# Optimization experiments

Hardware: AMD Instinct MI355X
Metric: run time of the kernel (lower is better)

The kernel has to match this reference:

```python
import jax, jax.numpy as jnp
import numpy as np
import math

B, S, E, H = 2, 2048, 1024, 16
D = E // H
# neuromodulator levels (deterministic branch choices)
NA, ACH, DA = 0.5, 0.5, -0.5

def setup_inputs() -> dict:
    key = jax.random.key(0)
    ks = jax.random.split(key, 12)
    xav = lambda k, i, o: jax.random.uniform(k, (i, o), jnp.float32, -1.0, 1.0) * math.sqrt(6.0 / (i + o))
    return {
        'query': jax.random.normal(ks[0], (B, S, E), jnp.float32),
        'key':   jax.random.normal(ks[1], (B, S, E), jnp.float32),
        'value': jax.random.normal(ks[2], (B, S, E), jnp.float32),
        'Wq': xav(ks[3], E, E), 'bq': jnp.zeros((E,), jnp.float32),
        'Wk': xav(ks[4], E, E), 'bk': jnp.zeros((E,), jnp.float32),
        'Wv': xav(ks[5], E, E), 'bv': jnp.zeros((E,), jnp.float32),
        'Wo': xav(ks[6], E, E), 'bo': jnp.zeros((E,), jnp.float32),
        'time_scales': jnp.ones((H,), jnp.float32),
    }

def reference(query, key, value, Wq, bq, Wk, bk, Wv, bv, Wo, bo, time_scales):
    # projections -> [B, H, S, D]
    q = (query @ Wq + bq).reshape(B, S, H, D).transpose(0, 2, 1, 3)
    k = (key   @ Wk + bk).reshape(B, S, H, D).transpose(0, 2, 1, 3)
    v = (value @ Wv + bv).reshape(B, S, H, D).transpose(0, 2, 1, 3)
    # per-head time-scale on keys
    k = k * time_scales[None, :, None, None]
    scores = jnp.einsum('bhtd,bhsd->bhts', q, k) / math.sqrt(D)
    # noradrenaline: temperature scaling
    temperature = 1.0 / (1.0 + NA * 0.5)
    scores = scores / temperature
    # acetylcholine: boost diagonal
    diag = jnp.eye(S, dtype=scores.dtype)[None, None]
    scores = scores * (1.0 + ACH * 0.3 * diag)
    kk = max(1, int(S * 0.2))
    topv = jax.lax.top_k(scores, kk)[0]          # [B,H,S,kk]
    min_topk = topv[..., -1:]                     # kth largest
    mask = (scores >= min_topk).astype(scores.dtype)
    scores = scores * (1.0 + (-DA) * 0.3 * mask)
    attn = jax.nn.softmax(scores, axis=-1)
    out = jnp.einsum('bhts,bhsd->bhtd', attn, v)
    out = out.transpose(0, 2, 1, 3).reshape(B, S, E)
    out = out @ Wo + bo
    return out
```

## Files before the change

### kernel.cpp

```cpp
#include <hip/hip_runtime.h>
#include <cstdint>
#include <cstddef>

#define BB 2
#define SS 2048
#define EE 1024
#define HH 16
#define DH 64
#define KKSEL 409
#define QT 16
#define PST 136

typedef __attribute__((ext_vector_type(8))) short bf16x8;
typedef __attribute__((ext_vector_type(4))) float f32x4;
typedef unsigned short ushort_t;

__device__ __forceinline__ unsigned short f2bf(float f){
    unsigned u = __float_as_uint(f);
    u += 0x7fffu + ((u >> 16) & 1u);
    return (unsigned short)(u >> 16);
}
__device__ __forceinline__ float bf2f(unsigned short h){
    return __uint_as_float(((unsigned)h) << 16);
}
__device__ __forceinline__ unsigned sortkey(float f){
    unsigned u = __float_as_uint(f);
    return (u & 0x80000000u) ? ~u : (u | 0x80000000u);
}
__device__ __forceinline__ float inv_sortkey(unsigned k){
    unsigned u = (k & 0x80000000u) ? (k & 0x7fffffffu) : ~k;
    return __uint_as_float(u);
}
__device__ __forceinline__ void split8(const float* f, bf16x8& h, bf16x8& l){
    #pragma unroll
    for (int j = 0; j < 8; ++j){
        ushort_t hh = f2bf(f[j]);
        h[j] = (short)hh;
        l[j] = (short)f2bf(f[j] - bf2f(hh));
    }
}

__global__ __launch_bounds__(256) void convert_wt(const float* __restrict__ W,
                                                  ushort_t* __restrict__ Ht,
                                                  ushort_t* __restrict__ Lt)
{
    __shared__ float T[64][65];
    const int tid = threadIdx.x;
    const int ty = tid >> 4, tx = tid & 15;
    const int n0 = blockIdx.x * 64, k0 = blockIdx.y * 64;
    #pragma unroll
    for (int i = 0; i < 4; ++i){
        const int kl = ty + i * 16;
        float4 w = *(const float4*)&W[(size_t)(k0 + kl) * EE + n0 + tx * 4];
        T[kl][tx*4 + 0] = w.x; T[kl][tx*4 + 1] = w.y;
        T[kl][tx*4 + 2] = w.z; T[kl][tx*4 + 3] = w.w;
    }
    __syncthreads();
    #pragma unroll
    for (int i = 0; i < 4; ++i){
        const int nl = ty + i * 16;
        ushort4 h, l;
        ushort_t* hp = &h.x; ushort_t* lp = &l.x;
        #pragma unroll
        for (int j = 0; j < 4; ++j){
            const float v = T[tx*4 + j][nl];
            ushort_t hh = f2bf(v);
            hp[j] = hh;
            lp[j] = f2bf(v - bf2f(hh));
        }
        const size_t o = (size_t)(n0 + nl) * EE + k0 + tx * 4;
        *(ushort4*)&Ht[o] = h;
        *(ushort4*)&Lt[o] = l;
    }
}

template<int MODE>
__global__ __launch_bounds__(256) void gemm_mfma(
        const float* __restrict__ X,
        const ushort_t* __restrict__ Wth, const ushort_t* __restrict__ Wtl,
        const float* __restrict__ bias, const float* __restrict__ ts,
        float* __restrict__ OutF, ushort_t* __restrict__ OutH,
        ushort_t* __restrict__ OutL)
{
    __shared__ ushort_t buf[2][16384];
    const int tid  = threadIdx.x;
    const int lane = tid & 63, wave = tid >> 6;
    const int c16  = lane & 15, qd = lane >> 4;
    const int m0 = blockIdx.y * 128, n0 = blockIdx.x * 128;
    const int wm = (wave >> 1) * 64, wn = (wave & 1) * 64;
    const int lrow = tid >> 1, lkg = (tid & 1) * 16;

    f32x4 acc[4][4];
    #pragma unroll
    for (int a = 0; a < 4; ++a)
        #pragma unroll
        for (int b = 0; b < 4; ++b) acc[a][b] = (f32x4){0.f,0.f,0.f,0.f};

    const float* Xr = X + (size_t)(m0 + lrow) * EE + lkg;
    const ushort_t* Whr = Wth + (size_t)(n0 + lrow) * EE + lkg;
    const ushort_t* Wlr = Wtl + (size_t)(n0 + lrow) * EE + lkg;

    {
        float fx[16];
        *(float4*)&fx[0]  = *(const float4*)&Xr[0];
        *(float4*)&fx[4]  = *(const float4*)&Xr[4];
        *(float4*)&fx[8]  = *(const float4*)&Xr[8];
        *(float4*)&fx[12] = *(const float4*)&Xr[12];
        bf16x8 w0 = *(const bf16x8*)&Whr[0];
        bf16x8 w1 = *(const bf16x8*)&Whr[8];
        bf16x8 w2 = *(const bf16x8*)&Wlr[0];
        bf16x8 w3 = *(const bf16x8*)&Wlr[8];
        bf16x8 h0, l0, h1, l1;
        split8(fx, h0, l0); split8(fx + 8, h1, l1);
        *(bf16x8*)&buf[0][lrow*32 + lkg]           = h0;
        *(bf16x8*)&buf[0][lrow*32 + lkg + 8]       = h1;
        *(bf16x8*)&buf[0][4096 + lrow*32 + lkg]    = l0;
        *(bf16x8*)&buf[0][4096 + lrow*32 + lkg+8]  = l1;
        *(bf16x8*)&buf[0][8192 + lrow*32 + lkg]    = w0;
        *(bf16x8*)&buf[0][8192 + lrow*32 + lkg+8]  = w1;
        *(bf16x8*)&buf[0][12288 + lrow*32 + lkg]   = w2;
        *(bf16x8*)&buf[0][12288 + lrow*32 + lkg+8] = w3;
    }
    __syncthreads();

    int cur = 0;
    for (int k0 = 0; k0 < EE; k0 += 32){
        const bool more = (k0 + 32) < EE;
        float fx[16];
        bf16x8 gw[4];
        if (more){
            const float* xp = Xr + k0 + 32;
            *(float4*)&fx[0]  = *(const float4*)&xp[0];
            *(float4*)&fx[4]  = *(const float4*)&xp[4];
            *(float4*)&fx[8]  = *(const float4*)&xp[8];
            *(float4*)&fx[12] = *(const float4*)&xp[12];
            gw[0] = *(const bf16x8*)&Whr[k0 + 32];
            gw[1] = *(const bf16x8*)&Whr[k0 + 40];
            gw[2] = *(const bf16x8*)&Wlr[k0 + 32];
            gw[3] = *(const bf16x8*)&Wlr[k0 + 40];
        }
        const ushort_t* A0 = &buf[cur][0];
        const ushort_t* A1 = &buf[cur][4096];
        const ushort_t* B0 = &buf[cur][8192];
        const ushort_t* B1 = &buf[cur][12288];
        bf16x8 afh[4], afl[4], bfh[4], bfl[4];
        #pragma unroll
        for (int i = 0; i < 4; ++i){
            afh[i] = *(const bf16x8*)&A0[(wm + i*16 + c16)*32 + qd*8];
            afl[i] = *(const bf16x8*)&A1[(wm + i*16 + c16)*32 + qd*8];
            bfh[i] = *(const bf16x8*)&B0[(wn + i*16 + c16)*32 + qd*8];
            bfl[i] = *(const bf16x8*)&B1[(wn + i*16 + c16)*32 + qd*8];
        }
        #pragma unroll
        for (int a = 0; a < 4; ++a){
            #pragma unroll
            for (int b = 0; b < 4; ++b){
                if (MODE == 2){
                    acc[a][b] = __builtin_amdgcn_mfma_f32_16x16x32_bf16(afh[a], bfh[b], acc[a][b], 0,0,0);
                    acc[a][b] = __builtin_amdgcn_mfma_f32_16x16x32_bf16(afh[a], bfl[b], acc[a][b], 0,0,0);
                    acc[a][b] = __builtin_amdgcn_mfma_f32_16x16x32_bf16(afl[a], bfh[b], acc[a][b], 0,0,0);
                } else {
                    acc[a][b] = __builtin_amdgcn_mfma_f32_16x16x32_bf16(bfh[a], afh[b], acc[a][b], 0,0,0);
                    acc[a][b] = __builtin_amdgcn_mfma_f32_16x16x32_bf16(bfh[a], afl[b], acc[a][b], 0,0,0);
                    acc[a][b] = __builtin_amdgcn_mfma_f32_16x16x32_bf16(bfl[a], afh[b], acc[a][b], 0,0,0);
                }
            }
        }
        if (more){
            bf16x8 h0, l0, h1, l1;
            split8(fx, h0, l0); split8(fx + 8, h1, l1);
            ushort_t* N = &buf[cur ^ 1][0];
            *(bf16x8*)&N[lrow*32 + lkg]           = h0;
            *(bf16x8*)&N[lrow*32 + lkg + 8]       = h1;
            *(bf16x8*)&N[4096 + lrow*32 + lkg]    = l0;
            *(bf16x8*)&N[4096 + lrow*32 + lkg+8]  = l1;
            *(bf16x8*)&N[8192 + lrow*32 + lkg]    = gw[0];
            *(bf16x8*)&N[8192 + lrow*32 + lkg+8]  = gw[1];
            *(bf16x8*)&N[12288 + lrow*32 + lkg]   = gw[2];
            *(bf16x8*)&N[12288 + lrow*32 + lkg+8] = gw[3];
            __syncthreads();
            cur ^= 1;
        }
    }

    if (MODE == 3){
        #pragma unroll
        for (int a = 0; a < 4; ++a){
            const int ng = n0 + wn + a*16 + qd*4;
            float4 b4 = *(const float4*)&bias[ng];
            const float bb[4] = {b4.x, b4.y, b4.z, b4.w};
            #pragma unroll
            for (int b = 0; b < 4; ++b){
                const int mg = m0 + wm + b*16 + c16;
                float4 o;
                o.x = acc[a][b][0] + bb[0]; o.y = acc[a][b][1] + bb[1];
                o.z = acc[a][b][2] + bb[2]; o.w = acc[a][b][3] + bb[3];
                *(float4*)&OutF[(size_t)mg * EE + ng] = o;
            }
        }
    } else if (MODE == 0){
        #pragma unroll
        for (int a = 0; a < 4; ++a){
            const int ng = n0 + wn + a*16 + qd*4;
            const int h = ng >> 6, d0 = ng & 63;
            float4 b4 = *(const float4*)&bias[ng];
            const float bb[4] = {b4.x, b4.y, b4.z, b4.w};
            #pragma unroll
            for (int b = 0; b < 4; ++b){
                const int mg = m0 + wm + b*16 + c16;
                const int bi = mg >> 11, s = mg & (SS - 1);
                ushort4 hv, lv;
                ushort_t* hp = &hv.x; ushort_t* lp = &lv.x;
                #pragma unroll
                for (int r = 0; r < 4; ++r){
                    const float v = acc[a][b][r] + bb[r];
                    ushort_t hh = f2bf(v);
                    hp[r] = hh;
                    lp[r] = f2bf(v - bf2f(hh));
                }
                const size_t o = (((size_t)(bi * HH + h)) * SS + s) * DH + d0;
                *(ushort4*)&OutH[o] = hv;
                *(ushort4*)&OutL[o] = lv;
            }
        }
    } else if (MODE == 1){
        #pragma unroll
        for (int a = 0; a < 4; ++a){
            const int ng = n0 + wn + a*16 + qd*4;
            const int h = ng >> 6, d0 = ng & 63;
            const float tsc = ts[h];
            float4 b4 = *(const float4*)&bias[ng];
            const float bb[4] = {b4.x, b4.y, b4.z, b4.w};
            #pragma unroll
            for (int b = 0; b < 4; ++b){
                const int mg = m0 + wm + b*16 + c16;
                const int bi = mg >> 11, s = mg & (SS - 1);
                ushort4 hv;
                ushort_t* hp = &hv.x;
                #pragma unroll
                for (int r = 0; r < 4; ++r)
                    hp[r] = f2bf((acc[a][b][r] + bb[r]) * tsc);
                *(ushort4*)&OutH[(((size_t)(bi * HH + h)) * SS + s) * DH + d0] = hv;
            }
        }
    } else {
        #pragma unroll
        for (int a = 0; a < 4; ++a){
            const int mg = m0 + wm + a*16 + qd*4;
            const int bi = mg >> 11, s0 = mg & (SS - 1);
            #pragma unroll
            for (int b = 0; b < 4; ++b){
                const int ng = n0 + wn + b*16 + c16;
                const int h = ng >> 6, d = ng & 63;
                const float bv = bias[ng];
                ushort4 hv;
                ushort_t* hp = &hv.x;
                #pragma unroll
                for (int r = 0; r < 4; ++r) hp[r] = f2bf(acc[a][b][r] + bv);
                *(ushort4*)&OutH[(((size_t)(bi * HH + h)) * DH + d) * SS + s0] = hv;
            }
        }
    }
}

__global__ __launch_bounds__(512, 4) void attn_kernel(
        const ushort_t* __restrict__ Qh, const ushort_t* __restrict__ Ql,
        const ushort_t* __restrict__ Khi, const ushort_t* __restrict__ Vth,
        float* __restrict__ AO)
{
    __shared__ __align__(16) char uni[65536];
    __shared__ float wsums[8][16];
    __shared__ unsigned thr16[16];

    const int tid  = threadIdx.x;
    const int lane = tid & 63;
    const int wave = tid >> 6;
    const int qd   = lane >> 4;
    const int c16  = lane & 15;
    const unsigned Bx = blockIdx.x;
    const int xcd  = Bx & 7;
    const int qq   = Bx >> 3;
    const int tile = qq & 127;
    const int bh   = (qq >> 7) * 8 + xcd;
    const int t0   = tile * QT;
    const int wbase = wave * 256;

    bf16x8 qh[2], ql[2];
    {
        const size_t qbase = ((size_t)bh * SS + t0 + c16) * DH;
        #pragma unroll
        for (int kc = 0; kc < 2; ++kc){
            qh[kc] = *(const bf16x8*)&Qh[qbase + kc*32 + qd*8];
            ql[kc] = *(const bf16x8*)&Ql[qbase + kc*32 + qd*8];
        }
    }

    f32x4 acc[16];
    const ushort_t* Kh = Khi + (size_t)bh * SS * DH;
    #pragma unroll
    for (int t = 0; t < 16; ++t){
        f32x4 a = {0.f, 0.f, 0.f, 0.f};
        const int srow = wbase + t*16 + c16;
        const ushort_t* kp = Kh + (size_t)srow * DH + qd*8;
        #pragma unroll
        for (int kc = 0; kc < 2; ++kc){
            bf16x8 kh = *(const bf16x8*)(kp + kc*32);
            a = __builtin_amdgcn_mfma_f32_16x16x32_bf16(qh[kc], kh, a, 0, 0, 0);
            a = __builtin_amdgcn_mfma_f32_16x16x32_bf16(ql[kc], kh, a, 0, 0, 0);
        }
        acc[t] = a;
    }

    #pragma unroll
    for (int t = 0; t < 16; ++t){
        const int colg = wbase + t*16 + c16;
        #pragma unroll
        for (int r = 0; r < 4; ++r){
            float v = acc[t][r] * 0.15625f;
            if (colg == t0 + qd*4 + r) v *= 1.15f;
            acc[t][r] = __uint_as_float(sortkey(v));
        }
    }

    float* ex = (float*)uni;
    #pragma unroll
    for (int half = 0; half < 2; ++half){
        if ((qd >> 1) == half){
            const int rl = (qd & 1) * 4;
            #pragma unroll
            for (int t = 0; t < 16; ++t)
                #pragma unroll
                for (int r = 0; r < 4; ++r)
                    ex[(rl + r) * SS + wbase + t*16 + c16] = acc[t][r];
        }
        __syncthreads();
        unsigned cand[32];
        #pragma unroll
        for (int j = 0; j < 32; ++j)
            cand[j] = __float_as_uint(ex[wave * SS + lane + 64*j]);
        unsigned lo = sortkey(-64.0f), hi = sortkey(64.0f);
        #pragma unroll 1
        for (int it = 0; it < 32; ++it){
            const unsigned mid = lo + ((hi - lo) >> 1);
            int c = 0;
            #pragma unroll
            for (int j = 0; j < 32; ++j){
                int pc;
                asm("v_cmp_le_u32 vcc, %1, %2\n\t"
                    "s_bcnt1_i32_b64 %0, vcc"
                    : "=s"(pc) : "s"(mid), "v"(cand[j]) : "vcc");
                c += pc;
            }
            if (c == KKSEL){ lo = mid; break; }
            if (c > KKSEL) lo = mid; else hi = mid;
        }
        if (lane == 0) thr16[half*8 + wave] = lo;
        __syncthreads();
    }

    unsigned thr[4];
    #pragma unroll
    for (int r = 0; r < 4; ++r) thr[r] = thr16[qd*4 + r];
    float psum[4] = {0.f, 0.f, 0.f, 0.f};
    #pragma unroll
    for (int t = 0; t < 16; ++t){
        #pragma unroll
        for (int r = 0; r < 4; ++r){
            const unsigned key = __float_as_uint(acc[t][r]);
            float s = inv_sortkey(key);
            s *= (key >= thr[r]) ? 1.15f : 1.0f;
            const float e = __expf(s);
            acc[t][r] = e;
            psum[r] += e;
        }
    }
    #pragma unroll
    for (int off = 1; off <= 8; off <<= 1){
        #pragma unroll
        for (int r = 0; r < 4; ++r) psum[r] += __shfl_xor(psum[r], off, 64);
    }
    if (c16 == 0){
        #pragma unroll
        for (int r = 0; r < 4; ++r) wsums[wave][qd*4 + r] = psum[r];
    }
    __syncthreads();
    float pinv[4];
    #pragma unroll
    for (int r = 0; r < 4; ++r){
        const int row = qd*4 + r;
        float s = 0.f;
        #pragma unroll
        for (int w = 0; w < 8; ++w) s += wsums[w][row];
        pinv[r] = 1.f / s;
    }

    const ushort_t* Vh = Vth + (size_t)bh * DH * SS;
    ushort_t* pw = (ushort_t*)uni + wave * (QT * PST);
    f32x4 oacc[4];
    #pragma unroll
    for (int dt = 0; dt < 4; ++dt) oacc[dt] = (f32x4){0.f, 0.f, 0.f, 0.f};

    #pragma unroll
    for (int half = 0; half < 2; ++half){
        #pragma unroll
        for (int tt = 0; tt < 8; ++tt){
            const int t = half*8 + tt;
            #pragma unroll
            for (int r = 0; r < 4; ++r)
                pw[(qd*4 + r) * PST + tt*16 + c16] = f2bf(acc[t][r] * pinv[r]);
        }
        #pragma unroll
        for (int kc = 0; kc < 4; ++kc){
            bf16x8 pf = *(const bf16x8*)&pw[c16 * PST + kc*32 + qd*8];
            const int sbase = wbase + half*128 + kc*32 + qd*8;
            #pragma unroll
            for (int dt = 0; dt < 4; ++dt){
                const int d = dt*16 + c16;
                bf16x8 vh = *(const bf16x8*)(Vh + (size_t)d * SS + sbase);
                oacc[dt] = __builtin_amdgcn_mfma_f32_16x16x32_bf16(pf, vh, oacc[dt], 0, 0, 0);
            }
        }
    }

    __syncthreads();
    float* red = (float*)uni;
    #pragma unroll
    for (int dt = 0; dt < 4; ++dt)
        #pragma unroll
        for (int r = 0; r < 4; ++r)
            red[(wave*16 + qd*4 + r) * 65 + dt*16 + c16] = oacc[dt][r];
    __syncthreads();

    const int b = bh >> 4, h = bh & 15;
    {
        const int r  = tid >> 5;
        const int c2 = (tid & 31) * 2;
        float s0 = 0.f, s1 = 0.f;
        #pragma unroll
        for (int w = 0; w < 8; ++w){
            s0 += red[(w*16 + r) * 65 + c2];
            s1 += red[(w*16 + r) * 65 + c2 + 1];
        }
        float2 o; o.x = s0; o.y = s1;
        *(float2*)&AO[((size_t)b * SS + t0 + r) * EE + h*DH + c2] = o;
    }
}

extern "C" void kernel_launch(void* const* d_in, const int* in_sizes, int n_in,
                              void* d_out, int out_size, void* d_ws, size_t ws_size,
                              hipStream_t stream)
{
    const float* query = (const float*)d_in[0];
    const float* key   = (const float*)d_in[1];
    const float* value = (const float*)d_in[2];
    const float* Wq    = (const float*)d_in[3];
    const float* bq    = (const float*)d_in[4];
    const float* Wk    = (const float*)d_in[5];
    const float* bk    = (const float*)d_in[6];
    const float* Wv    = (const float*)d_in[7];
    const float* bv    = (const float*)d_in[8];
    const float* Wo    = (const float*)d_in[9];
    const float* bo    = (const float*)d_in[10];
    const float* ts    = (const float*)d_in[11];
    float* out = (float*)d_out;
    char* w = (char*)d_ws;

    const size_t MB = 1u << 20;
    ushort_t* Qh  = (ushort_t*)(w + 0 * MB);
    ushort_t* Ql  = (ushort_t*)(w + 8 * MB);
    ushort_t* Kh  = (ushort_t*)(w + 16 * MB);
    ushort_t* Vth = (ushort_t*)(w + 24 * MB);
    float*    AOw = (float*)   (w + 32 * MB);
    ushort_t* Wth = (ushort_t*)(w + 48 * MB);
    ushort_t* Wtl = (ushort_t*)(w + 50 * MB);

    dim3 cb(256);
    dim3 wtg(16, 16);
    dim3 gg(8, 32), gb(256);

    hipLaunchKernelGGL(convert_wt, wtg, cb, 0, stream, Wq, Wth, Wtl);
    hipLaunchKernelGGL((gemm_mfma<0>), gg, gb, 0, stream, query, Wth, Wtl, bq, nullptr,
                       nullptr, Qh, Ql);
    hipLaunchKernelGGL(convert_wt, wtg, cb, 0, stream, Wk, Wth, Wtl);
    hipLaunchKernelGGL((gemm_mfma<1>), gg, gb, 0, stream, key, Wth, Wtl, bk, ts,
                       nullptr, Kh, nullptr);
    hipLaunchKernelGGL(convert_wt, wtg, cb, 0, stream, Wv, Wth, Wtl);
    hipLaunchKernelGGL((gemm_mfma<2>), gg, gb, 0, stream, value, Wth, Wtl, bv, nullptr,
                       nullptr, Vth, nullptr);
    hipLaunchKernelGGL(attn_kernel, dim3(BB * HH * (SS / QT)), dim3(512), 0, stream,
                       Qh, Ql, Kh, Vth, AOw);
    hipLaunchKernelGGL(convert_wt, wtg, cb, 0, stream, Wo, Wth, Wtl);
    hipLaunchKernelGGL((gemm_mfma<3>), gg, gb, 0, stream, AOw, Wth, Wtl, bo, nullptr,
                       out, nullptr, nullptr);
}
```

Before: 700.3 us.

## Batch weight conversion and QKV GEMMs into single launches; narrow top-k threshold search

All four weight transpose/split conversions now run in one launch, each into its own buffer. The three Q/K/V projection GEMMs run as one grid with a z dimension, so the GPU gets three times as many blocks at once and there are fewer launches and serial gaps. The attention top-k threshold search now keeps raw float scores and starts its binary search from each row's min/max. It exits early once the interval collapses, and counts with a ballot on float comparisons. The converted Q/K/V weights reuse the attention-output workspace region, which relies on them being dead before attention writes its output.

New measurement: 656.4 us. 1.07x faster.

```diff
diff --git a/kernel.cpp b/kernel.cpp
--- a/kernel.cpp
+++ b/kernel.cpp
@@ -40,11 +40,20 @@
     }
 }
 
-__global__ __launch_bounds__(256) void convert_wt(const float* __restrict__ W,
-                                                  ushort_t* __restrict__ Ht,
-                                                  ushort_t* __restrict__ Lt)
+struct CvtArgs {
+    const float* W[4];
+    ushort_t* H[4];
+    ushort_t* L[4];
+};
+
+__global__ __launch_bounds__(256) void convert_wt4(CvtArgs a)
 {
     __shared__ float T[64][65];
+    const int z = blockIdx.z;
+    const float* __restrict__ W = a.W[z];
+    ushort_t* __restrict__ Ht = a.H[z];
+    ushort_t* __restrict__ Lt = a.L[z];
+
     const int tid = threadIdx.x;
     const int ty = tid >> 4, tx = tid & 15;
     const int n0 = blockIdx.x * 64, k0 = blockIdx.y * 64;
@@ -75,14 +84,13 @@
 }
 
 template<int MODE>
-__global__ __launch_bounds__(256) void gemm_mfma(
+__device__ __forceinline__ void gemm_body(
         const float* __restrict__ X,
         const ushort_t* __restrict__ Wth, const ushort_t* __restrict__ Wtl,
         const float* __restrict__ bias, const float* __restrict__ ts,
         float* __restrict__ OutF, ushort_t* __restrict__ OutH,
-        ushort_t* __restrict__ OutL)
+        ushort_t* __restrict__ OutL, ushort_t* buf)
 {
-    __shared__ ushort_t buf[2][16384];
     const int tid  = threadIdx.x;
     const int lane = tid & 63, wave = tid >> 6;
     const int c16  = lane & 15, qd = lane >> 4;
@@ -112,14 +120,15 @@
         bf16x8 w3 = *(const bf16x8*)&Wlr[8];
         bf16x8 h0, l0, h1, l1;
         split8(fx, h0, l0); split8(fx + 8, h1, l1);
-        *(bf16x8*)&buf[0][lrow*32 + lkg]           = h0;
-        *(bf16x8*)&buf[0][lrow*32 + lkg + 8]       = h1;
-        *(bf16x8*)&buf[0][4096 + lrow*32 + lkg]    = l0;
-        *(bf16x8*)&buf[0][4096 + lrow*32 + lkg+8]  = l1;
-        *(bf16x8*)&buf[0][8192 + lrow*32 + lkg]    = w0;
-        *(bf16x8*)&buf[0][8192 + lrow*32 + lkg+8]  = w1;
-        *(bf16x8*)&buf[0][12288 + lrow*32 + lkg]   = w2;
-        *(bf16x8*)&buf[0][12288 + lrow*32 + lkg+8] = w3;
+        ushort_t* S = buf;
+        *(bf16x8*)&S[lrow*32 + lkg]           = h0;
+        *(bf16x8*)&S[lrow*32 + lkg + 8]       = h1;
+        *(bf16x8*)&S[4096 + lrow*32 + lkg]    = l0;
+        *(bf16x8*)&S[4096 + lrow*32 + lkg+8]  = l1;
+        *(bf16x8*)&S[8192 + lrow*32 + lkg]    = w0;
+        *(bf16x8*)&S[8192 + lrow*32 + lkg+8]  = w1;
+        *(bf16x8*)&S[12288 + lrow*32 + lkg]   = w2;
+        *(bf16x8*)&S[12288 + lrow*32 + lkg+8] = w3;
     }
     __syncthreads();
 
@@ -139,10 +148,11 @@
             gw[2] = *(const bf16x8*)&Wlr[k0 + 32];
             gw[3] = *(const bf16x8*)&Wlr[k0 + 40];
         }
-        const ushort_t* A0 = &buf[cur][0];
-        const ushort_t* A1 = &buf[cur][4096];
-        const ushort_t* B0 = &buf[cur][8192];
-        const ushort_t* B1 = &buf[cur][12288];
+        const ushort_t* S  = buf + cur * 16384;
+        const ushort_t* A0 = S;
+        const ushort_t* A1 = S + 4096;
+        const ushort_t* B0 = S + 8192;
+        const ushort_t* B1 = S + 12288;
         bf16x8 afh[4], afl[4], bfh[4], bfl[4];
         #pragma unroll
         for (int i = 0; i < 4; ++i){
@@ -169,7 +179,7 @@
         if (more){
             bf16x8 h0, l0, h1, l1;
             split8(fx, h0, l0); split8(fx + 8, h1, l1);
-            ushort_t* N = &buf[cur ^ 1][0];
+            ushort_t* N = buf + (cur ^ 1) * 16384;
             *(bf16x8*)&N[lrow*32 + lkg]           = h0;
             *(bf16x8*)&N[lrow*32 + lkg + 8]       = h1;
             *(bf16x8*)&N[4096 + lrow*32 + lkg]    = l0;
@@ -263,6 +273,36 @@
     }
 }
 
+__global__ __launch_bounds__(256) void gemm_qkv(
+        const float* __restrict__ q, const float* __restrict__ k,
+        const float* __restrict__ v,
+        const ushort_t* __restrict__ Wqh, const ushort_t* __restrict__ Wql,
+        const ushort_t* __restrict__ Wkh, const ushort_t* __restrict__ Wkl,
+        const ushort_t* __restrict__ Wvh, const ushort_t* __restrict__ Wvl,
+        const float* __restrict__ bq, const float* __restrict__ bk,
+        const float* __restrict__ bv, const float* __restrict__ ts,
+        ushort_t* __restrict__ Qh, ushort_t* __restrict__ Ql,
+        ushort_t* __restrict__ Kh, ushort_t* __restrict__ Vth)
+{
+    __shared__ ushort_t buf[2 * 16384];
+    const int z = blockIdx.z;
+    if (z == 0)
+        gemm_body<0>(q, Wqh, Wql, bq, nullptr, nullptr, Qh, Ql, buf);
+    else if (z == 1)
+        gemm_body<1>(k, Wkh, Wkl, bk, ts, nullptr, Kh, nullptr, buf);
+    else
+        gemm_body<2>(v, Wvh, Wvl, bv, nullptr, nullptr, Vth, nullptr, buf);
+}
+
+__global__ __launch_bounds__(256) void gemm_out(
+        const float* __restrict__ X,
+        const ushort_t* __restrict__ Wth, const ushort_t* __restrict__ Wtl,
+        const float* __restrict__ bias, float* __restrict__ OutF)
+{
+    __shared__ ushort_t buf[2 * 16384];
+    gemm_body<3>(X, Wth, Wtl, bias, nullptr, OutF, nullptr, nullptr, buf);
+}
+
 __global__ __launch_bounds__(512, 4) void attn_kernel(
         const ushort_t* __restrict__ Qh, const ushort_t* __restrict__ Ql,
         const ushort_t* __restrict__ Khi, const ushort_t* __restrict__ Vth,
@@ -270,7 +310,7 @@
 {
     __shared__ __align__(16) char uni[65536];
     __shared__ float wsums[8][16];
-    __shared__ unsigned thr16[16];
+    __shared__ float thr16[16];
 
     const int tid  = threadIdx.x;
     const int lane = tid & 63;
@@ -318,7 +358,7 @@
         for (int r = 0; r < 4; ++r){
             float v = acc[t][r] * 0.15625f;
             if (colg == t0 + qd*4 + r) v *= 1.15f;
-            acc[t][r] = __uint_as_float(sortkey(v));
+            acc[t][r] = v;
         }
     }
 
@@ -334,31 +374,38 @@
                     ex[(rl + r) * SS + wbase + t*16 + c16] = acc[t][r];
         }
         __syncthreads();
-        unsigned cand[32];
+        float cand[32];
         #pragma unroll
         for (int j = 0; j < 32; ++j)
-            cand[j] = __float_as_uint(ex[wave * SS + lane + 64*j]);
-        unsigned lo = sortkey(-64.0f), hi = sortkey(64.0f);
+            cand[j] = ex[wave * SS + lane + 64*j];
+        float mx = cand[0], mn = cand[0];
+        #pragma unroll
+        for (int j = 1; j < 32; ++j){
+            mx = fmaxf(mx, cand[j]);
+            mn = fminf(mn, cand[j]);
+        }
+        #pragma unroll
+        for (int off = 1; off < 64; off <<= 1){
+            mx = fmaxf(mx, __shfl_xor(mx, off, 64));
+            mn = fminf(mn, __shfl_xor(mn, off, 64));
+        }
+        unsigned lo = sortkey(mn), hi = sortkey(mx) + 1u;
         #pragma unroll 1
-        for (int it = 0; it < 32; ++it){
+        for (int it = 0; it < 32 && (hi - lo) > 1u; ++it){
             const unsigned mid = lo + ((hi - lo) >> 1);
+            const float midf = inv_sortkey(mid);
             int c = 0;
             #pragma unroll
-            for (int j = 0; j < 32; ++j){
-                int pc;
-                asm("v_cmp_le_u32 vcc, %1, %2\n\t"
-                    "s_bcnt1_i32_b64 %0, vcc"
-                    : "=s"(pc) : "s"(mid), "v"(cand[j]) : "vcc");
-                c += pc;
-            }
+            for (int j = 0; j < 32; ++j)
+                c += (int)__popcll(__ballot(cand[j] >= midf));
             if (c == KKSEL){ lo = mid; break; }
             if (c > KKSEL) lo = mid; else hi = mid;
         }
-        if (lane == 0) thr16[half*8 + wave] = lo;
+        if (lane == 0) thr16[half*8 + wave] = inv_sortkey(lo);
         __syncthreads();
     }
 
-    unsigned thr[4];
+    float thr[4];
     #pragma unroll
     for (int r = 0; r < 4; ++r) thr[r] = thr16[qd*4 + r];
     float psum[4] = {0.f, 0.f, 0.f, 0.f};
@@ -366,9 +413,8 @@
     for (int t = 0; t < 16; ++t){
         #pragma unroll
         for (int r = 0; r < 4; ++r){
-            const unsigned key = __float_as_uint(acc[t][r]);
-            float s = inv_sortkey(key);
-            s *= (key >= thr[r]) ? 1.15f : 1.0f;
+            float s = acc[t][r];
+            s *= (s >= thr[r]) ? 1.15f : 1.0f;
             const float e = __expf(s);
             acc[t][r] = e;
             psum[r] += e;
@@ -471,25 +517,26 @@
     ushort_t* Kh  = (ushort_t*)(w + 16 * MB);
     ushort_t* Vth = (ushort_t*)(w + 24 * MB);
     float*    AOw = (float*)   (w + 32 * MB);
-    ushort_t* Wth = (ushort_t*)(w + 48 * MB);
-    ushort_t* Wtl = (ushort_t*)(w + 50 * MB);
-
-    dim3 cb(256);
-    dim3 wtg(16, 16);
-    dim3 gg(8, 32), gb(256);
-
-    hipLaunchKernelGGL(convert_wt, wtg, cb, 0, stream, Wq, Wth, Wtl);
-    hipLaunchKernelGGL((gemm_mfma<0>), gg, gb, 0, stream, query, Wth, Wtl, bq, nullptr,
-                       nullptr, Qh, Ql);
-    hipLaunchKernelGGL(convert_wt, wtg, cb, 0, stream, Wk, Wth, Wtl);
-    hipLaunchKernelGGL((gemm_mfma<1>), gg, gb, 0, stream, key, Wth, Wtl, bk, ts,
-                       nullptr, Kh, nullptr);
-    hipLaunchKernelGGL(convert_wt, wtg, cb, 0, stream, Wv, Wth, Wtl);
-    hipLaunchKernelGGL((gemm_mfma<2>), gg, gb, 0, stream, value, Wth, Wtl, bv, nullptr,
-                       nullptr, Vth, nullptr);
+    ushort_t* Wqh = (ushort_t*)(w + 32 * MB);
+    ushort_t* Wql = (ushort_t*)(w + 34 * MB);
+    ushort_t* Wkh = (ushort_t*)(w + 36 * MB);
+    ushort_t* Wkl = (ushort_t*)(w + 38 * MB);
+    ushort_t* Wvh = (ushort_t*)(w + 40 * MB);
+    ushort_t* Wvl = (ushort_t*)(w + 42 * MB);
+    ushort_t* Woh = (ushort_t*)(w + 48 * MB);
+    ushort_t* Wol = (ushort_t*)(w + 50 * MB);
+
+    CvtArgs ca;
+    ca.W[0] = Wq;  ca.W[1] = Wk;  ca.W[2] = Wv;  ca.W[3] = Wo;
+    ca.H[0] = Wqh; ca.H[1] = Wkh; ca.H[2] = Wvh; ca.H[3] = Woh;
+    ca.L[0] = Wql; ca.L[1] = Wkl; ca.L[2] = Wvl; ca.L[3] = Wol;
+
+    hipLaunchKernelGGL(convert_wt4, dim3(16, 16, 4), dim3(256), 0, stream, ca);
+    hipLaunchKernelGGL(gemm_qkv, dim3(8, 32, 3), dim3(256), 0, stream,
+                       query, key, value, Wqh, Wql, Wkh, Wkl, Wvh, Wvl,
+                       bq, bk, bv, ts, Qh, Ql, Kh, Vth);
     hipLaunchKernelGGL(attn_kernel, dim3(BB * HH * (SS / QT)), dim3(512), 0, stream,
                        Qh, Ql, Kh, Vth, AOw);
-    hipLaunchKernelGGL(convert_wt, wtg, cb, 0, stream, Wo, Wth, Wtl);
-    hipLaunchKernelGGL((gemm_mfma<3>), gg, gb, 0, stream, AOw, Wth, Wtl, bo, nullptr,
-                       out, nullptr, nullptr);
-}
+    hipLaunchKernelGGL(gemm_out, dim3(8, 32), dim3(256), 0, stream,
+                       AOw, Woh, Wol, bo, out);
+}
```
